# Kernel tuning notes

Measured on AMD Instinct MI355X. Metric: run time of the kernel, lower is better.

Reference implementation:

```python
import math
import jax, jax.numpy as jnp
import numpy as np

B, H, Nt, Nl, E = 4, 16, 512, 512, 64
P = H * E  # 1024, pre-projection embedding dim


def setup_inputs() -> dict:
    key = jax.random.key(0)
    ks = jax.random.split(key, 8)
    return {
        "projected_u": jax.random.normal(ks[0], (B, H, Nt, P), jnp.float32),
        "projected_b": jax.random.normal(ks[1], (B, H, Nt, 1), jnp.float32),
        "mu": jax.random.normal(ks[2], (B, Nl, P), jnp.float32),
        "logvar": jax.random.normal(ks[3], (B, Nl, P), jnp.float32) * 0.5,
        "pi": jax.random.uniform(ks[4], (B, Nl, 1), jnp.float32, 1e-3, 1.0),
        "w_v": jax.random.normal(ks[5], (H, E, P), jnp.float32) * 0.02,
        "b_v": jax.random.normal(ks[6], (H, E, Nl), jnp.float32) * 0.02,
        "attn_mask": jnp.zeros((B * H, 1, Nl), dtype=bool),  # True = masked
    }


def reference(projected_u, projected_b, mu, logvar, pi, w_v, b_v, attn_mask):
    Bq, Hq, Ntq, Pq = projected_u.shape
    Nlq = mu.shape[1]
    Eq = w_v.shape[1]
    prior_var_u = math.sqrt(Eq)

    var = jnp.exp(logvar)                         # [B,Nl,P]
    biased_var = var + prior_var_u                # [B,Nl,P]

    # float additive mask [B*H,1,Nl]: -inf where attn_mask True or pi<=0
    pi_rep = jnp.repeat(pi, Hq, axis=0)           # [B*H,Nl,1]
    am = jnp.where(attn_mask, -jnp.inf, 0.0)
    am = am + jnp.where(pi_rep.transpose(0, 2, 1) <= 0, -jnp.inf, 0.0)
    masked = jnp.isneginf(am).transpose(0, 2, 1)  # [B*H,Nl,1]

    # scores [B,H,Nt,Nl]
    attn = jnp.einsum('bhmp,bnp->bhmn', projected_u, mu / biased_var) + projected_b

    pi_c = jnp.maximum(pi_rep, jnp.finfo(pi_rep.dtype).tiny)
    t1 = jnp.where(masked, 0.0, jnp.log(pi_c))                                  # [B*H,Nl,1]
    t2 = 0.5 * jnp.sum((mu / jnp.sqrt(biased_var)) ** 2, axis=-1, keepdims=True)  # [B,Nl,1]
    t2 = jnp.repeat(t2, Hq, axis=0)                                             # [B*H,Nl,1]
    t3 = jnp.where(masked, 0.0, jnp.log(jnp.repeat(biased_var, Hq, axis=0)))    # [B*H,Nl,P]
    t3 = jnp.sum(0.5 * t3, axis=-1, keepdims=True)                              # [B*H,Nl,1]

    attn = attn + (t1 - t2 - t3).reshape(Bq, Hq, Nlq, 1).transpose(0, 1, 3, 2)  # [B,H,1,Nl]
    attn = attn + am.reshape(Bq, Hq, 1, Nlq)
    attn = jax.nn.softmax(attn, axis=-1)                                        # [B,H,Nt,Nl]

    # denoised values: interpolation between query projection and means
    out = (jnp.einsum('bhmn,bnp->bhmp', attn, var / biased_var) * projected_u
           + jnp.einsum('bhmn,bnp->bhmp', attn, (prior_var_u / biased_var) * mu))  # [B,H,Nt,P]
    out = (jnp.einsum('bhmp,hep->bhme', out, w_v)
           + jnp.einsum('bhmn,hen->bhme', attn, b_v))                              # [B,H,Nt,E]
    return (out.reshape(Bq * Hq, Ntq, Eq), attn.reshape(Bq * Hq, Ntq, Nlq))
```

## Files before the change

kernel.cpp:

```cpp
#include <hip/hip_runtime.h>
#include <cstdint>
#include <cstddef>
#include <cmath>

#define B_  4
#define H_  16
#define NT  512
#define NL  512
#define E_  64
#define P_  1024
#define HE  1024
#define BH  64

typedef __attribute__((ext_vector_type(8))) short short8;
typedef __attribute__((ext_vector_type(4))) float f32x4;
typedef unsigned short u16;

#define MFMA(a, b, c) __builtin_amdgcn_mfma_f32_16x16x32_bf16(a, b, c, 0, 0, 0)

static __device__ inline u16 f2bf_rne(float f) {
  unsigned u = __float_as_uint(f);
  unsigned r = u + 0x7FFFu + ((u >> 16) & 1u);
  return (u16)(r >> 16);
}

static __device__ inline void gl_lds16(const void* g, void* l) {
  __builtin_amdgcn_global_load_lds(
      (const __attribute__((address_space(1))) void*)g,
      (__attribute__((address_space(3))) void*)l, 16, 0, 0);
}

__global__ __launch_bounds__(256) void k_precompute(
    const float* __restrict__ mu, const float* __restrict__ logvar,
    const float* __restrict__ pi, u16* __restrict__ mobv_hi,
    u16* __restrict__ mobv_lo, u16* __restrict__ ibvT,
    float* __restrict__ bias) {
  const int bn = blockIdx.x;
  const int b = bn >> 9, n = bn & 511;
  const int t = threadIdx.x;
  const size_t base = (size_t)bn * P_;
  float t2 = 0.f, t3 = 0.f;
#pragma unroll
  for (int i = 0; i < P_ / 256; ++i) {
    const int p = t + i * 256;
    const float lv  = logvar[base + p];
    const float v   = expf(lv);
    const float bv  = v + 8.0f;
    const float inv = 1.0f / bv;
    const float m   = mu[base + p];
    const float x   = m * inv;
    const unsigned bits = __float_as_uint(x);
    mobv_hi[base + p] = (u16)(bits >> 16);
    const float r = x - __uint_as_float(bits & 0xFFFF0000u);
    mobv_lo[base + p] = (u16)(__float_as_uint(r) >> 16);
    ibvT[((size_t)b * P_ + p) * NL + n] = f2bf_rne(inv);
    t2 += m * x;
    t3 += logf(bv);
  }
  __shared__ float r2[256];
  __shared__ float r3[256];
  r2[t] = t2; r3[t] = t3;
  __syncthreads();
  for (int s = 128; s > 0; s >>= 1) {
    if (t < s) { r2[t] += r2[t + s]; r3[t] += r3[t + s]; }
    __syncthreads();
  }
  if (t == 0) {
    const float pv = pi[bn];
    float bb;
    if (pv <= 0.f) bb = -INFINITY;
    else bb = logf(fmaxf(pv, 1.17549435e-38f)) - 0.5f * r2[0] - 0.5f * r3[0];
    bias[bn] = bb;
  }
}

__global__ __launch_bounds__(256) void k_wvcast(const float* __restrict__ wv,
                                                u16* __restrict__ wvb) {
  const int i = (blockIdx.x * 256 + threadIdx.x) * 4;
  const float4 f = *(const float4*)&wv[i];
  wvb[i + 0] = f2bf_rne(f.x);
  wvb[i + 1] = f2bf_rne(f.y);
  wvb[i + 2] = f2bf_rne(f.z);
  wvb[i + 3] = f2bf_rne(f.w);
}

__global__ __launch_bounds__(256) void k_w2p(
    const u16* __restrict__ mobv_hi, const u16* __restrict__ mobv_lo,
    const u16* __restrict__ wvb, const float* __restrict__ bv_,
    u16* __restrict__ W2pT) {
  const int b    = blockIdx.z;
  const int row0 = blockIdx.x * 64;
  const int col0 = blockIdx.y * 128;
  const int t = threadIdx.x;
  const int wave = t >> 6, lane = t & 63;
  const int l16 = lane & 15, sel = lane >> 4;
  const int mrow = (wave >> 1) * 32, ncol = (wave & 1) * 64;

  __shared__ u16 Ah[64 * 32];
  __shared__ u16 Al[64 * 32];
  __shared__ u16 Bs[128 * 32];

  const u16* Abh = mobv_hi + ((size_t)b * NL + row0) * P_;
  const u16* Abl = mobv_lo + ((size_t)b * NL + row0) * P_;
  const u16* Bb  = wvb + (size_t)col0 * P_;

  f32x4 acc[2][4];
#pragma unroll
  for (int i = 0; i < 2; ++i)
#pragma unroll
    for (int j = 0; j < 4; ++j) acc[i][j] = (f32x4){0.f, 0.f, 0.f, 0.f};

  for (int k0 = 0; k0 < P_; k0 += 32) {
    {
      const int c = t;
      const int row = c >> 2, k8 = (c & 3) ^ ((row >> 1) & 3);
      gl_lds16(Abh + (size_t)row * P_ + k0 + k8 * 8, &Ah[wave * 64 * 8]);
      gl_lds16(Abl + (size_t)row * P_ + k0 + k8 * 8, &Al[wave * 64 * 8]);
    }
#pragma unroll
    for (int i = 0; i < 2; ++i) {
      const int c = t + i * 256;
      const int row = c >> 2, k8 = (c & 3) ^ ((row >> 1) & 3);
      gl_lds16(Bb + (size_t)row * P_ + k0 + k8 * 8,
               &Bs[(i * 256 + wave * 64) * 8]);
    }
    __syncthreads();
    short8 ah[2], al[2], bf[4];
#pragma unroll
    for (int mt = 0; mt < 2; ++mt) {
      const int r = mrow + mt * 16 + l16;
      const int ch = sel ^ ((r >> 1) & 3);
      ah[mt] = *(const short8*)&Ah[r * 32 + ch * 8];
      al[mt] = *(const short8*)&Al[r * 32 + ch * 8];
    }
#pragma unroll
    for (int nt = 0; nt < 4; ++nt) {
      const int r = ncol + nt * 16 + l16;
      const int ch = sel ^ ((r >> 1) & 3);
      bf[nt] = *(const short8*)&Bs[r * 32 + ch * 8];
    }
#pragma unroll
    for (int mt = 0; mt < 2; ++mt)
#pragma unroll
      for (int nt = 0; nt < 4; ++nt) {
        acc[mt][nt] = MFMA(ah[mt], bf[nt], acc[mt][nt]);
        acc[mt][nt] = MFMA(al[mt], bf[nt], acc[mt][nt]);
      }
    __syncthreads();
  }
#pragma unroll
  for (int mt = 0; mt < 2; ++mt) {
    const int nbase = row0 + mrow + mt * 16 + sel * 4;
#pragma unroll
    for (int nt = 0; nt < 4; ++nt) {
      const int he = col0 + ncol + nt * 16 + l16;
      const float4 bvv = *(const float4*)&bv_[(size_t)he * NL + nbase];
      ushort4 o;
      o.x = f2bf_rne(8.0f * acc[mt][nt][0] + bvv.x);
      o.y = f2bf_rne(8.0f * acc[mt][nt][1] + bvv.y);
      o.z = f2bf_rne(8.0f * acc[mt][nt][2] + bvv.z);
      o.w = f2bf_rne(8.0f * acc[mt][nt][3] + bvv.w);
      *(ushort4*)&W2pT[((size_t)b * HE + he) * NL + nbase] = o;
    }
  }
}

__global__ __launch_bounds__(256) void k_scores(
    const float* __restrict__ U, const u16* __restrict__ mobv_hi,
    const u16* __restrict__ mobv_lo, const float* __restrict__ pb,
    const float* __restrict__ bias, const uint8_t* __restrict__ mask,
    float* __restrict__ attn) {
  const int b    = blockIdx.z;
  const int row0 = blockIdx.x * 128;
  const int col0 = blockIdx.y * 128;
  const int t = threadIdx.x;
  const int wave = t >> 6, lane = t & 63;
  const int l16 = lane & 15, sel = lane >> 4;
  const int mrow = (wave >> 1) * 64, ncol = (wave & 1) * 64;

  __shared__ float Af[2][128 * 32];
  __shared__ u16   Bh[2][128 * 32];
  __shared__ u16   Bl[2][128 * 32];

  const float* Ab  = U + ((size_t)b * 8192 + row0) * P_;
  const u16*   Bbh = mobv_hi + ((size_t)b * NL + col0) * P_;
  const u16*   Bbl = mobv_lo + ((size_t)b * NL + col0) * P_;

  f32x4 acc[4][4];
#pragma unroll
  for (int i = 0; i < 4; ++i)
#pragma unroll
    for (int j = 0; j < 4; ++j) acc[i][j] = (f32x4){0.f, 0.f, 0.f, 0.f};

  auto stage = [&](int buf, int k0) {
#pragma unroll
    for (int i = 0; i < 4; ++i) {
      const int c = t + i * 256;
      const int row = c >> 3, k4 = (c & 7) ^ (row & 7);
      gl_lds16(Ab + (size_t)row * P_ + k0 + k4 * 4,
               &Af[buf][(i * 256 + wave * 64) * 4]);
    }
#pragma unroll
    for (int i = 0; i < 2; ++i) {
      const int c = t + i * 256;
      const int row = c >> 2, k8 = (c & 3) ^ ((row >> 1) & 3);
      gl_lds16(Bbh + (size_t)row * P_ + k0 + k8 * 8,
               &Bh[buf][(i * 256 + wave * 64) * 8]);
      gl_lds16(Bbl + (size_t)row * P_ + k0 + k8 * 8,
               &Bl[buf][(i * 256 + wave * 64) * 8]);
    }
  };

  stage(0, 0);
  __syncthreads();
  int cur = 0;
  for (int k0 = 0; k0 < P_; k0 += 32) {
    if (k0 + 32 < P_) stage(cur ^ 1, k0 + 32);

    short8 ah[4], al[4], bh[4], bl[4];
#pragma unroll
    for (int mt = 0; mt < 4; ++mt) {
      const int r = mrow + mt * 16 + l16;
      const int c0 = (sel * 2) ^ (r & 7);
      const int c1 = (sel * 2 + 1) ^ (r & 7);
      const float4 f0 = *(const float4*)&Af[cur][r * 32 + c0 * 4];
      const float4 f1 = *(const float4*)&Af[cur][r * 32 + c1 * 4];
      const float fv[8] = {f0.x, f0.y, f0.z, f0.w, f1.x, f1.y, f1.z, f1.w};
#pragma unroll
      for (int j = 0; j < 8; ++j) {
        const unsigned bits = __float_as_uint(fv[j]);
        ah[mt][j] = (short)(bits >> 16);
        const float rr = fv[j] - __uint_as_float(bits & 0xFFFF0000u);
        al[mt][j] = (short)(__float_as_uint(rr) >> 16);
      }
    }
#pragma unroll
    for (int nt = 0; nt < 4; ++nt) {
      const int r = ncol + nt * 16 + l16;
      const int ch = sel ^ ((r >> 1) & 3);
      bh[nt] = *(const short8*)&Bh[cur][r * 32 + ch * 8];
      bl[nt] = *(const short8*)&Bl[cur][r * 32 + ch * 8];
    }
#pragma unroll
    for (int mt = 0; mt < 4; ++mt)
#pragma unroll
      for (int nt = 0; nt < 4; ++nt) {
        acc[mt][nt] = MFMA(ah[mt], bh[nt], acc[mt][nt]);
        acc[mt][nt] = MFMA(ah[mt], bl[nt], acc[mt][nt]);
        acc[mt][nt] = MFMA(al[mt], bh[nt], acc[mt][nt]);
      }
    __syncthreads();
    cur ^= 1;
  }

  const int bh_ = b * H_ + (row0 >> 9);
  float pbv[4][4];
#pragma unroll
  for (int mt = 0; mt < 4; ++mt)
#pragma unroll
    for (int r = 0; r < 4; ++r)
      pbv[mt][r] = pb[(size_t)b * 8192 + row0 + mrow + mt * 16 + sel * 4 + r];
#pragma unroll
  for (int nt = 0; nt < 4; ++nt) {
    const int n = col0 + ncol + nt * 16 + l16;
    const float bcol = bias[b * NL + n];
    const bool mk = mask[(size_t)bh_ * NL + n] != 0;
#pragma unroll
    for (int mt = 0; mt < 4; ++mt) {
#pragma unroll
      for (int r = 0; r < 4; ++r) {
        const int row = row0 + mrow + mt * 16 + sel * 4 + r;
        float s = acc[mt][nt][r] + pbv[mt][r] + bcol;
        if (mk) s = -INFINITY;
        attn[((size_t)b * 8192 + row) * NL + n] = s;
      }
    }
  }
}

__global__ __launch_bounds__(256) void k_softmax(float* __restrict__ attn,
                                                 u16* __restrict__ attn_bf) {
  const int t = threadIdx.x;
  const int wave = t >> 6, lane = t & 63;
  const size_t r = (size_t)blockIdx.x * 4 + wave;
  float* row = attn + r * NL;
  const float4 v0 = ((const float4*)row)[lane * 2];
  const float4 v1 = ((const float4*)row)[lane * 2 + 1];
  float m = fmaxf(fmaxf(fmaxf(v0.x, v0.y), fmaxf(v0.z, v0.w)),
                  fmaxf(fmaxf(v1.x, v1.y), fmaxf(v1.z, v1.w)));
#pragma unroll
  for (int off = 32; off > 0; off >>= 1) m = fmaxf(m, __shfl_xor(m, off, 64));
  float e[8];
  e[0] = expf(v0.x - m); e[1] = expf(v0.y - m);
  e[2] = expf(v0.z - m); e[3] = expf(v0.w - m);
  e[4] = expf(v1.x - m); e[5] = expf(v1.y - m);
  e[6] = expf(v1.z - m); e[7] = expf(v1.w - m);
  float s = ((e[0] + e[1]) + (e[2] + e[3])) + ((e[4] + e[5]) + (e[6] + e[7]));
#pragma unroll
  for (int off = 32; off > 0; off >>= 1) s += __shfl_xor(s, off, 64);
  const float inv = 1.0f / s;
  float4 o0, o1;
  o0.x = e[0] * inv; o0.y = e[1] * inv; o0.z = e[2] * inv; o0.w = e[3] * inv;
  o1.x = e[4] * inv; o1.y = e[5] * inv; o1.z = e[6] * inv; o1.w = e[7] * inv;
  ((float4*)row)[lane * 2] = o0;
  ((float4*)row)[lane * 2 + 1] = o1;
  ushort4 b0, b1;
  b0.x = f2bf_rne(o0.x); b0.y = f2bf_rne(o0.y);
  b0.z = f2bf_rne(o0.z); b0.w = f2bf_rne(o0.w);
  b1.x = f2bf_rne(o1.x); b1.y = f2bf_rne(o1.y);
  b1.z = f2bf_rne(o1.z); b1.w = f2bf_rne(o1.w);
  ((ushort4*)(attn_bf + r * NL))[lane * 2] = b0;
  ((ushort4*)(attn_bf + r * NL))[lane * 2 + 1] = b1;
}

__global__ __launch_bounds__(256) void k_mid(
    const u16* __restrict__ attn_bf, const u16* __restrict__ ibvT,
    const float* __restrict__ U, u16* __restrict__ opS) {
  const int b    = blockIdx.z;
  const int row0 = blockIdx.x * 128;
  const int col0 = blockIdx.y * 128;
  const int t = threadIdx.x;
  const int wave = t >> 6, lane = t & 63;
  const int l16 = lane & 15, sel = lane >> 4;
  const int mrow = (wave >> 1) * 64, ncol = (wave & 1) * 64;

  __shared__ u16 As[2][128 * 32];
  __shared__ u16 Bs[2][128 * 32];

  const u16* Ab = attn_bf + ((size_t)b * 8192 + row0) * NL;
  const u16* Bb = ibvT + ((size_t)b * P_ + col0) * NL;

  f32x4 acc[4][4];
#pragma unroll
  for (int i = 0; i < 4; ++i)
#pragma unroll
    for (int j = 0; j < 4; ++j) acc[i][j] = (f32x4){0.f, 0.f, 0.f, 0.f};

  auto stage = [&](int buf, int k0) {
#pragma unroll
    for (int i = 0; i < 2; ++i) {
      const int c = t + i * 256;
      const int row = c >> 2, k8 = (c & 3) ^ ((row >> 1) & 3);
      gl_lds16(Ab + (size_t)row * NL + k0 + k8 * 8,
               &As[buf][(i * 256 + wave * 64) * 8]);
      gl_lds16(Bb + (size_t)row * NL + k0 + k8 * 8,
               &Bs[buf][(i * 256 + wave * 64) * 8]);
    }
  };

  stage(0, 0);
  __syncthreads();
  int cur = 0;
  for (int k0 = 0; k0 < NL; k0 += 32) {
    if (k0 + 32 < NL) stage(cur ^ 1, k0 + 32);
    short8 af[4], bf[4];
#pragma unroll
    for (int mt = 0; mt < 4; ++mt) {
      const int r = mrow + mt * 16 + l16;
      const int ch = sel ^ ((r >> 1) & 3);
      af[mt] = *(const short8*)&As[cur][r * 32 + ch * 8];
    }
#pragma unroll
    for (int nt = 0; nt < 4; ++nt) {
      const int r = ncol + nt * 16 + l16;
      const int ch = sel ^ ((r >> 1) & 3);
      bf[nt] = *(const short8*)&Bs[cur][r * 32 + ch * 8];
    }
#pragma unroll
    for (int mt = 0; mt < 4; ++mt)
#pragma unroll
      for (int nt = 0; nt < 4; ++nt)
        acc[mt][nt] = MFMA(af[mt], bf[nt], acc[mt][nt]);
    __syncthreads();
    cur ^= 1;
  }

#pragma unroll
  for (int mt = 0; mt < 4; ++mt) {
#pragma unroll
    for (int r = 0; r < 4; ++r) {
      const int m = row0 + mrow + mt * 16 + sel * 4 + r;
      const float* Urow = U + ((size_t)b * 8192 + m) * P_;
      u16* orow = opS + ((size_t)b * 8192 + m) * P_;
#pragma unroll
      for (int nt = 0; nt < 4; ++nt) {
        const int p = col0 + ncol + nt * 16 + l16;
        const float u = Urow[p];
        orow[p] = f2bf_rne((1.0f - 8.0f * acc[mt][nt][r]) * u);
      }
    }
  }
}

__global__ __launch_bounds__(256) void k_out2(
    const u16* __restrict__ opS, const u16* __restrict__ attn_bf,
    const u16* __restrict__ wvb, const u16* __restrict__ W2pT,
    float* __restrict__ out) {
  const int bh = blockIdx.y;
  const int b = bh >> 4, h = bh & 15;
  const int row0g = bh * NT + blockIdx.x * 64;
  const int t = threadIdx.x;
  const int wave = t >> 6, lane = t & 63;
  const int l16 = lane & 15, sel = lane >> 4;
  const int mrow = (wave >> 1) * 32, ncol = (wave & 1) * 32;

  __shared__ u16 As[64 * 64];
  __shared__ u16 Bs[64 * 64];

  f32x4 acc[2][2];
#pragma unroll
  for (int i = 0; i < 2; ++i)
#pragma unroll
    for (int j = 0; j < 2; ++j) acc[i][j] = (f32x4){0.f, 0.f, 0.f, 0.f};

  const u16* Ab1 = opS + (size_t)row0g * P_;
  const u16* Bb1 = wvb + (size_t)(h * 64) * P_;
  for (int k0 = 0; k0 < P_; k0 += 64) {
#pragma unroll
    for (int i = 0; i < 2; ++i) {
      const int c = t + i * 256;
      const int row = c >> 3, k8 = (c & 7) ^ (row & 7);
      gl_lds16(Ab1 + (size_t)row * P_ + k0 + k8 * 8,
               &As[(i * 256 + wave * 64) * 8]);
      gl_lds16(Bb1 + (size_t)row * P_ + k0 + k8 * 8,
               &Bs[(i * 256 + wave * 64) * 8]);
    }
    __syncthreads();
    short8 af[2][2], bf[2][2];
#pragma unroll
    for (int mt = 0; mt < 2; ++mt) {
      const int r = mrow + mt * 16 + l16;
#pragma unroll
      for (int kk = 0; kk < 2; ++kk) {
        const int ch = (kk * 4 + sel) ^ (r & 7);
        af[mt][kk] = *(const short8*)&As[r * 64 + ch * 8];
      }
    }
#pragma unroll
    for (int nt = 0; nt < 2; ++nt) {
      const int r = ncol + nt * 16 + l16;
#pragma unroll
      for (int kk = 0; kk < 2; ++kk) {
        const int ch = (kk * 4 + sel) ^ (r & 7);
        bf[nt][kk] = *(const short8*)&Bs[r * 64 + ch * 8];
      }
    }
#pragma unroll
    for (int mt = 0; mt < 2; ++mt)
#pragma unroll
      for (int nt = 0; nt < 2; ++nt) {
        acc[mt][nt] = MFMA(af[mt][0], bf[nt][0], acc[mt][nt]);
        acc[mt][nt] = MFMA(af[mt][1], bf[nt][1], acc[mt][nt]);
      }
    __syncthreads();
  }

  const u16* Ab2 = attn_bf + (size_t)row0g * NL;
  const u16* Bb2 = W2pT + ((size_t)b * HE + h * 64) * NL;
  for (int k0 = 0; k0 < NL; k0 += 64) {
#pragma unroll
    for (int i = 0; i < 2; ++i) {
      const int c = t + i * 256;
      const int row = c >> 3, k8 = (c & 7) ^ (row & 7);
      gl_lds16(Ab2 + (size_t)row * NL + k0 + k8 * 8,
               &As[(i * 256 + wave * 64) * 8]);
      gl_lds16(Bb2 + (size_t)row * NL + k0 + k8 * 8,
               &Bs[(i * 256 + wave * 64) * 8]);
    }
    __syncthreads();
    short8 af[2][2], bf[2][2];
#pragma unroll
    for (int mt = 0; mt < 2; ++mt) {
      const int r = mrow + mt * 16 + l16;
#pragma unroll
      for (int kk = 0; kk < 2; ++kk) {
        const int ch = (kk * 4 + sel) ^ (r & 7);
        af[mt][kk] = *(const short8*)&As[r * 64 + ch * 8];
      }
    }
#pragma unroll
    for (int nt = 0; nt < 2; ++nt) {
      const int r = ncol + nt * 16 + l16;
#pragma unroll
      for (int kk = 0; kk < 2; ++kk) {
        const int ch = (kk * 4 + sel) ^ (r & 7);
        bf[nt][kk] = *(const short8*)&Bs[r * 64 + ch * 8];
      }
    }
#pragma unroll
    for (int mt = 0; mt < 2; ++mt)
#pragma unroll
      for (int nt = 0; nt < 2; ++nt) {
        acc[mt][nt] = MFMA(af[mt][0], bf[nt][0], acc[mt][nt]);
        acc[mt][nt] = MFMA(af[mt][1], bf[nt][1], acc[mt][nt]);
      }
    __syncthreads();
  }

#pragma unroll
  for (int mt = 0; mt < 2; ++mt)
#pragma unroll
    for (int nt = 0; nt < 2; ++nt)
#pragma unroll
      for (int r = 0; r < 4; ++r) {
        const int row = row0g + mrow + mt * 16 + sel * 4 + r;
        const int e = ncol + nt * 16 + l16;
        out[(size_t)row * E_ + e] = acc[mt][nt][r];
      }
}

extern "C" void kernel_launch(void* const* d_in, const int* in_sizes, int n_in,
                              void* d_out, int out_size, void* d_ws, size_t ws_size,
                              hipStream_t stream) {
  const float*   u    = (const float*)d_in[0];
  const float*   pb   = (const float*)d_in[1];
  const float*   mu   = (const float*)d_in[2];
  const float*   logv = (const float*)d_in[3];
  const float*   pi   = (const float*)d_in[4];
  const float*   wv   = (const float*)d_in[5];
  const float*   bv   = (const float*)d_in[6];
  const uint8_t* mask = (const uint8_t*)d_in[7];

  float* out  = (float*)d_out;
  float* attn = out + (size_t)BH * NT * E_;

  u16*   mobv_hi = (u16*)d_ws;
  u16*   mobv_lo = mobv_hi + (size_t)B_ * NL * P_;
  u16*   ibvT    = mobv_lo + (size_t)B_ * NL * P_;
  u16*   W2pT    = ibvT + (size_t)B_ * P_ * NL;
  u16*   wvb     = W2pT + (size_t)B_ * HE * NL;
  float* bias    = (float*)(wvb + (size_t)HE * P_);
  u16*   attn_bf = (u16*)(bias + (size_t)B_ * NL);
  u16*   opS     = attn_bf + (size_t)BH * NT * NL;

  k_precompute<<<B_ * NL, 256, 0, stream>>>(mu, logv, pi, mobv_hi, mobv_lo,
                                            ibvT, bias);
  k_wvcast<<<(HE * P_) / 1024, 256, 0, stream>>>(wv, wvb);
  k_w2p<<<dim3(NL / 64, HE / 128, B_), 256, 0, stream>>>(mobv_hi, mobv_lo, wvb,
                                                         bv, W2pT);
  k_scores<<<dim3(8192 / 128, NL / 128, B_), 256, 0, stream>>>(
      u, mobv_hi, mobv_lo, pb, bias, mask, attn);
  k_softmax<<<(B_ * H_ * NT) / 4, 256, 0, stream>>>(attn, attn_bf);
  k_mid<<<dim3(8192 / 128, P_ / 128, B_), 256, 0, stream>>>(attn_bf, ibvT, u,
                                                            opS);
  k_out2<<<dim3(NT / 64, BH), 256, 0, stream>>>(opS, attn_bf, wvb, W2pT, out);
}
```

Before: 510.0 us.

## Add separate transpose kernel, reshape scores wave tiling, single-buffer mid kernel

```diff
diff --git a/kernel.cpp b/kernel.cpp
--- a/kernel.cpp
+++ b/kernel.cpp
@@ -13,6 +13,7 @@
 #define BH  64
 
 typedef __attribute__((ext_vector_type(8))) short short8;
+typedef __attribute__((ext_vector_type(8))) unsigned short ushort8;
 typedef __attribute__((ext_vector_type(4))) float f32x4;
 typedef unsigned short u16;
 
@@ -33,10 +34,9 @@
 __global__ __launch_bounds__(256) void k_precompute(
     const float* __restrict__ mu, const float* __restrict__ logvar,
     const float* __restrict__ pi, u16* __restrict__ mobv_hi,
-    u16* __restrict__ mobv_lo, u16* __restrict__ ibvT,
+    u16* __restrict__ mobv_lo, u16* __restrict__ ibv,
     float* __restrict__ bias) {
   const int bn = blockIdx.x;
-  const int b = bn >> 9, n = bn & 511;
   const int t = threadIdx.x;
   const size_t base = (size_t)bn * P_;
   float t2 = 0.f, t3 = 0.f;
@@ -53,7 +53,7 @@
     mobv_hi[base + p] = (u16)(bits >> 16);
     const float r = x - __uint_as_float(bits & 0xFFFF0000u);
     mobv_lo[base + p] = (u16)(__float_as_uint(r) >> 16);
-    ibvT[((size_t)b * P_ + p) * NL + n] = f2bf_rne(inv);
+    ibv[base + p] = f2bf_rne(inv);
     t2 += m * x;
     t3 += logf(bv);
   }
@@ -71,6 +71,33 @@
     if (pv <= 0.f) bb = -INFINITY;
     else bb = logf(fmaxf(pv, 1.17549435e-38f)) - 0.5f * r2[0] - 0.5f * r3[0];
     bias[bn] = bb;
+  }
+}
+
+__global__ __launch_bounds__(256) void k_tr(const u16* __restrict__ ibv,
+                                            u16* __restrict__ ibvT) {
+  const int b  = blockIdx.z;
+  const int p0 = blockIdx.x * 64;
+  const int n0 = blockIdx.y * 64;
+  const int t  = threadIdx.x;
+  __shared__ u16 T[64][65];
+  {
+    const int ln = t >> 2, lp = (t & 3) * 16;
+    const u16* src = ibv + ((size_t)b * NL + n0 + ln) * P_ + p0 + lp;
+    const ushort8 v0 = *(const ushort8*)(src);
+    const ushort8 v1 = *(const ushort8*)(src + 8);
+#pragma unroll
+    for (int j = 0; j < 8; ++j) { T[ln][lp + j] = v0[j]; T[ln][lp + 8 + j] = v1[j]; }
+  }
+  __syncthreads();
+  {
+    const int lp = t >> 2, ln = (t & 3) * 16;
+    u16* dst = ibvT + ((size_t)b * P_ + p0 + lp) * NL + n0 + ln;
+    ushort8 o0, o1;
+#pragma unroll
+    for (int j = 0; j < 8; ++j) { o0[j] = T[ln + j][lp]; o1[j] = T[ln + 8 + j][lp]; }
+    *(ushort8*)(dst)     = o0;
+    *(ushort8*)(dst + 8) = o1;
   }
 }
 
@@ -176,7 +203,7 @@
   const int t = threadIdx.x;
   const int wave = t >> 6, lane = t & 63;
   const int l16 = lane & 15, sel = lane >> 4;
-  const int mrow = (wave >> 1) * 64, ncol = (wave & 1) * 64;
+  const int mrow = wave * 32;
 
   __shared__ float Af[2][128 * 32];
   __shared__ u16   Bh[2][128 * 32];
@@ -186,11 +213,11 @@
   const u16*   Bbh = mobv_hi + ((size_t)b * NL + col0) * P_;
   const u16*   Bbl = mobv_lo + ((size_t)b * NL + col0) * P_;
 
-  f32x4 acc[4][4];
-#pragma unroll
-  for (int i = 0; i < 4; ++i)
-#pragma unroll
-    for (int j = 0; j < 4; ++j) acc[i][j] = (f32x4){0.f, 0.f, 0.f, 0.f};
+  f32x4 acc[2][8];
+#pragma unroll
+  for (int i = 0; i < 2; ++i)
+#pragma unroll
+    for (int j = 0; j < 8; ++j) acc[i][j] = (f32x4){0.f, 0.f, 0.f, 0.f};
 
   auto stage = [&](int buf, int k0) {
 #pragma unroll
@@ -217,9 +244,9 @@
   for (int k0 = 0; k0 < P_; k0 += 32) {
     if (k0 + 32 < P_) stage(cur ^ 1, k0 + 32);
 
-    short8 ah[4], al[4], bh[4], bl[4];
-#pragma unroll
-    for (int mt = 0; mt < 4; ++mt) {
+    short8 ah[2], al[2], bh[8], bl[8];
+#pragma unroll
+    for (int mt = 0; mt < 2; ++mt) {
       const int r = mrow + mt * 16 + l16;
       const int c0 = (sel * 2) ^ (r & 7);
       const int c1 = (sel * 2 + 1) ^ (r & 7);
@@ -235,16 +262,16 @@
       }
     }
 #pragma unroll
-    for (int nt = 0; nt < 4; ++nt) {
-      const int r = ncol + nt * 16 + l16;
+    for (int nt = 0; nt < 8; ++nt) {
+      const int r = nt * 16 + l16;
       const int ch = sel ^ ((r >> 1) & 3);
       bh[nt] = *(const short8*)&Bh[cur][r * 32 + ch * 8];
       bl[nt] = *(const short8*)&Bl[cur][r * 32 + ch * 8];
     }
 #pragma unroll
-    for (int mt = 0; mt < 4; ++mt)
-#pragma unroll
-      for (int nt = 0; nt < 4; ++nt) {
+    for (int mt = 0; mt < 2; ++mt)
+#pragma unroll
+      for (int nt = 0; nt < 8; ++nt) {
         acc[mt][nt] = MFMA(ah[mt], bh[nt], acc[mt][nt]);
         acc[mt][nt] = MFMA(ah[mt], bl[nt], acc[mt][nt]);
         acc[mt][nt] = MFMA(al[mt], bh[nt], acc[mt][nt]);
@@ -254,19 +281,19 @@
   }
 
   const int bh_ = b * H_ + (row0 >> 9);
-  float pbv[4][4];
-#pragma unroll
-  for (int mt = 0; mt < 4; ++mt)
+  float pbv[2][4];
+#pragma unroll
+  for (int mt = 0; mt < 2; ++mt)
 #pragma unroll
     for (int r = 0; r < 4; ++r)
       pbv[mt][r] = pb[(size_t)b * 8192 + row0 + mrow + mt * 16 + sel * 4 + r];
 #pragma unroll
-  for (int nt = 0; nt < 4; ++nt) {
-    const int n = col0 + ncol + nt * 16 + l16;
+  for (int nt = 0; nt < 8; ++nt) {
+    const int n = col0 + nt * 16 + l16;
     const float bcol = bias[b * NL + n];
     const bool mk = mask[(size_t)bh_ * NL + n] != 0;
 #pragma unroll
-    for (int mt = 0; mt < 4; ++mt) {
+    for (int mt = 0; mt < 2; ++mt) {
 #pragma unroll
       for (int r = 0; r < 4; ++r) {
         const int row = row0 + mrow + mt * 16 + sel * 4 + r;
@@ -324,8 +351,8 @@
   const int l16 = lane & 15, sel = lane >> 4;
   const int mrow = (wave >> 1) * 64, ncol = (wave & 1) * 64;
 
-  __shared__ u16 As[2][128 * 32];
-  __shared__ u16 Bs[2][128 * 32];
+  __shared__ u16 As[128 * 32];
+  __shared__ u16 Bs[128 * 32];
 
   const u16* Ab = attn_bf + ((size_t)b * 8192 + row0) * NL;
   const u16* Bb = ibvT + ((size_t)b * P_ + col0) * NL;
@@ -336,35 +363,29 @@
 #pragma unroll
     for (int j = 0; j < 4; ++j) acc[i][j] = (f32x4){0.f, 0.f, 0.f, 0.f};
 
-  auto stage = [&](int buf, int k0) {
+  for (int k0 = 0; k0 < NL; k0 += 32) {
 #pragma unroll
     for (int i = 0; i < 2; ++i) {
       const int c = t + i * 256;
       const int row = c >> 2, k8 = (c & 3) ^ ((row >> 1) & 3);
       gl_lds16(Ab + (size_t)row * NL + k0 + k8 * 8,
-               &As[buf][(i * 256 + wave * 64) * 8]);
+               &As[(i * 256 + wave * 64) * 8]);
       gl_lds16(Bb + (size_t)row * NL + k0 + k8 * 8,
-               &Bs[buf][(i * 256 + wave * 64) * 8]);
-    }
-  };
-
-  stage(0, 0);
-  __syncthreads();
-  int cur = 0;
-  for (int k0 = 0; k0 < NL; k0 += 32) {
-    if (k0 + 32 < NL) stage(cur ^ 1, k0 + 32);
+               &Bs[(i * 256 + wave * 64) * 8]);
+    }
+    __syncthreads();
     short8 af[4], bf[4];
 #pragma unroll
     for (int mt = 0; mt < 4; ++mt) {
       const int r = mrow + mt * 16 + l16;
       const int ch = sel ^ ((r >> 1) & 3);
-      af[mt] = *(const short8*)&As[cur][r * 32 + ch * 8];
+      af[mt] = *(const short8*)&As[r * 32 + ch * 8];
     }
 #pragma unroll
     for (int nt = 0; nt < 4; ++nt) {
       const int r = ncol + nt * 16 + l16;
       const int ch = sel ^ ((r >> 1) & 3);
-      bf[nt] = *(const short8*)&Bs[cur][r * 32 + ch * 8];
+      bf[nt] = *(const short8*)&Bs[r * 32 + ch * 8];
     }
 #pragma unroll
     for (int mt = 0; mt < 4; ++mt)
@@ -372,7 +393,6 @@
       for (int nt = 0; nt < 4; ++nt)
         acc[mt][nt] = MFMA(af[mt], bf[nt], acc[mt][nt]);
     __syncthreads();
-    cur ^= 1;
   }
 
 #pragma unroll
@@ -532,9 +552,11 @@
   float* bias    = (float*)(wvb + (size_t)HE * P_);
   u16*   attn_bf = (u16*)(bias + (size_t)B_ * NL);
   u16*   opS     = attn_bf + (size_t)BH * NT * NL;
+  u16*   ibv     = opS;
 
   k_precompute<<<B_ * NL, 256, 0, stream>>>(mu, logv, pi, mobv_hi, mobv_lo,
-                                            ibvT, bias);
+                                            ibv, bias);
+  k_tr<<<dim3(P_ / 64, NL / 64, B_), 256, 0, stream>>>(ibv, ibvT);
   k_wvcast<<<(HE * P_) / 1024, 256, 0, stream>>>(wv, wvb);
   k_w2p<<<dim3(NL / 64, HE / 128, B_), 256, 0, stream>>>(mobv_hi, mobv_lo, wvb,
                                                          bv, W2pT);
```

New measurement: 464.9 us. -8.8%, faster.
